# Kernel optimization log

Hardware: AMD Instinct MI355X
Metric: run time of the kernel (lower is better)

Reference implementation:

```python
import jax, jax.numpy as jnp
import numpy as np

N, D, M, H, L, FF = 24, 128, 9, 8, 2, 256
F = D // H  # head dim = 16


def _ln(x, g, b, eps=1e-5):
    mu = jnp.mean(x, -1, keepdims=True)
    var = jnp.mean((x - mu) ** 2, -1, keepdims=True)
    return (x - mu) * jax.lax.rsqrt(var + eps) * g + b


def _pos_encoding(T, d):
    pos = np.arange(T)[:, None].astype(np.float32)
    div = np.exp(np.arange(0, d, 2).astype(np.float32) * (-np.log(10000.0) / d))
    pe = np.zeros((T, d), np.float32)
    pe[:, 0::2] = np.sin(pos * div)
    pe[:, 1::2] = np.cos(pos * div)
    return jnp.asarray(pe)


def _forward(inputs, emb_W, emb_b, sa_Wq, sa_bq, sa_Wk, sa_bk, sa_Wv, sa_bv,
             ta_Wq, ta_bq, ta_Wk, ta_bk, ta_Wv, ta_bv, ta_Wo, ta_bo,
             ln_g, ln_b, lns_g, lns_b, ff_W1, ff_b1, ff_W2, ff_b2, fin_W, fin_b):
    B, T, _ = inputs.shape
    # joint embedding: per-joint linear M->D
    x4 = inputs.reshape(B, T, N, M)
    emb = jnp.einsum('btnm,nmd->btnd', x4, emb_W) + emb_b
    x = emb.reshape(B, T, N * D) + _pos_encoding(T, N * D)[None]
    x = x.transpose(1, 0, 2)  # (T, B, N*D)
    # faithful to source: float attn_mask = tril(ones, -1) is ADDED to scores in torch MHA
    mask = jnp.tril(jnp.ones((T, T), x.dtype), -1)
    inv_sF = 1.0 / np.sqrt(F).astype(np.float32)
    for l in range(L):
        xl = x.reshape(T, B, N, D)
        # ---- spatial attention: K,V shared across joints, Q per joint, per head ----
        Ksp = jnp.einsum('tbnd,hdf->tbhnf', xl, sa_Wk[l]) + sa_bk[l][:, None, :]
        Vsp = jnp.einsum('tbnd,hdf->tbhnf', xl, sa_Wv[l]) + sa_bv[l][:, None, :]
        Qsp = jnp.einsum('tbnd,hndf->tbhnf', xl, sa_Wq[l]) + sa_bq[l]
        Asp = jax.nn.softmax(jnp.einsum('tbhnf,tbhmf->tbhnm', Qsp, Ksp) * inv_sF, axis=-1)
        so = jnp.einsum('tbhnm,tbhmf->tbhnf', Asp, Vsp)
        spatial = so.transpose(0, 1, 3, 2, 4).reshape(T, B, N * D)  # concat heads per joint
        spatial = _ln(spatial + x, ln_g[l], ln_b[l])
        # ---- temporal attention: independent MHA per joint (batched over joints) ----
        q = (jnp.einsum('tbnd,nde->tbne', xl, ta_Wq[l]) + ta_bq[l]).reshape(T, B, N, H, F)
        k = (jnp.einsum('tbnd,nde->tbne', xl, ta_Wk[l]) + ta_bk[l]).reshape(T, B, N, H, F)
        v = (jnp.einsum('tbnd,nde->tbne', xl, ta_Wv[l]) + ta_bv[l]).reshape(T, B, N, H, F)
        sc = jnp.einsum('tbnhf,sbnhf->bnhts', q, k) * inv_sF + mask
        At = jax.nn.softmax(sc, axis=-1)
        to = jnp.einsum('bnhts,sbnhf->tbnhf', At, v).reshape(T, B, N, D)
        to = jnp.einsum('tbnd,nde->tbne', to, ta_Wo[l]) + ta_bo[l]
        temporal = _ln(to.reshape(T, B, N * D) + x, ln_g[l], ln_b[l])
        # ---- per-joint feed-forward + residual + small layernorm ----
        a = (spatial + temporal).reshape(T, B, N, D)
        ff = jax.nn.relu(jnp.einsum('tbnd,df->tbnf', a, ff_W1[l]) + ff_b1[l])
        ff = jnp.einsum('tbnf,fd->tbnd', ff, ff_W2[l]) + ff_b2[l]
        x = _ln(ff + a, lns_g[l], lns_b[l]).reshape(T, B, N * D)
    o = jnp.einsum('tbnd,dm->tbnm', x.reshape(T, B, N, D), fin_W) + fin_b
    return o.reshape(T, B, N * M).transpose(1, 0, 2) + inputs


def setup_inputs() -> dict:
    key = jax.random.key(0)
    ks = jax.random.split(key, 20)
    s = 0.05
    rn = lambda k, shape: jax.random.normal(k, shape, jnp.float32) * s
    return {
        'inputs': jax.random.normal(ks[0], (16, 192, N * M), jnp.float32),
        'emb_W': rn(ks[1], (N, M, D)), 'emb_b': rn(ks[2], (N, D)),
        'sa_Wq': rn(ks[3], (L, H, N, D, F)), 'sa_bq': rn(ks[4], (L, H, N, F)),
        'sa_Wk': rn(ks[5], (L, H, D, F)), 'sa_bk': rn(ks[6], (L, H, F)),
        'sa_Wv': rn(ks[7], (L, H, D, F)), 'sa_bv': rn(ks[8], (L, H, F)),
        'ta_Wq': rn(ks[9], (L, N, D, D)), 'ta_bq': rn(ks[10], (L, N, D)),
        'ta_Wk': rn(ks[11], (L, N, D, D)), 'ta_bk': rn(ks[12], (L, N, D)),
        'ta_Wv': rn(ks[13], (L, N, D, D)), 'ta_bv': rn(ks[14], (L, N, D)),
        'ta_Wo': rn(ks[15], (L, N, D, D)), 'ta_bo': jnp.zeros((L, N, D), jnp.float32),
        'ln_g': jnp.ones((L, N * D), jnp.float32), 'ln_b': jnp.zeros((L, N * D), jnp.float32),
        'lns_g': jnp.ones((L, D), jnp.float32), 'lns_b': jnp.zeros((L, D), jnp.float32),
        'ff_W1': rn(ks[16], (L, D, FF)), 'ff_b1': jnp.zeros((L, FF), jnp.float32),
        'ff_W2': rn(ks[17], (L, FF, D)), 'ff_b2': jnp.zeros((L, D), jnp.float32),
        'fin_W': rn(ks[18], (D, M)), 'fin_b': jnp.zeros((M,), jnp.float32),
    }


def reference(inputs, emb_W, emb_b, sa_Wq, sa_bq, sa_Wk, sa_bk, sa_Wv, sa_bv,
              ta_Wq, ta_bq, ta_Wk, ta_bk, ta_Wv, ta_bv, ta_Wo, ta_bo,
              ln_g, ln_b, lns_g, lns_b, ff_W1, ff_b1, ff_W2, ff_b2, fin_W, fin_b):
    return _forward(inputs, emb_W, emb_b, sa_Wq, sa_bq, sa_Wk, sa_bk, sa_Wv, sa_bv,
                    ta_Wq, ta_bq, ta_Wk, ta_bk, ta_Wv, ta_bv, ta_Wo, ta_bo,
                    ln_g, ln_b, lns_g, lns_b, ff_W1, ff_b1, ff_W2, ff_b2, fin_W, fin_b)
```

## Files before the change

### kernel.cpp

```cpp
#include <hip/hip_runtime.h>
#include <cmath>

namespace {
constexpr int B_ = 16, T_ = 192, N_ = 24, D_ = 128, M_ = 9, H_ = 8, F_ = 16, FF_ = 256;
constexpr int ND_ = N_ * D_;
constexpr int ROWS_ = T_ * B_;
constexpr long long SZ_ = (long long)ROWS_ * ND_;
constexpr long long WL_ = 2064384;
}

typedef __attribute__((ext_vector_type(8))) short bf16x8_t;
typedef __attribute__((ext_vector_type(4))) short bf16x4_t;
typedef __attribute__((ext_vector_type(4))) float f32x4_t;

static __device__ __forceinline__ ushort f2bf(float f) {
  union { float f; uint u; } v; v.f = f;
  uint r = v.u + 0x7fffu + ((v.u >> 16) & 1u);
  return (ushort)(r >> 16);
}
static __device__ __forceinline__ float bf2f(ushort u) {
  union { uint u; float f; } v; v.u = ((uint)u) << 16; return v.f;
}
static __device__ __forceinline__ bf16x4_t cvt4(f32x4_t x) {
  bf16x4_t r;
  r[0] = (short)f2bf(x[0]); r[1] = (short)f2bf(x[1]);
  r[2] = (short)f2bf(x[2]); r[3] = (short)f2bf(x[3]);
  return r;
}

__global__ __launch_bounds__(256) void k_pe(float* __restrict__ pe)
{
  int i = blockIdx.x * 256 + threadIdx.x;
  if (i >= T_ * ND_) return;
  int t = i / ND_, c = i % ND_;
  float freq = expf((float)(2 * (c >> 1)) * (-9.210340371976184f / 3072.0f));
  float ang = (float)t * freq;
  pe[i] = (c & 1) ? cosf(ang) : sinf(ang);
}

__global__ __launch_bounds__(256) void k_embed(const float* __restrict__ in,
                                               const float* __restrict__ Wemb,
                                               const float* __restrict__ bemb,
                                               const float* __restrict__ pe,
                                               ushort* __restrict__ Xb)
{
  int row = blockIdx.x;
  int t = row / B_, b = row % B_;
  int tid = threadIdx.x;
  __shared__ float inr[N_ * M_];
  const float* ip = in + ((size_t)b * T_ + t) * (N_ * M_);
  if (tid < N_ * M_) inr[tid] = ip[tid];
  __syncthreads();
  uint* Xr = (uint*)(Xb + (size_t)row * ND_);
  const float* per = pe + (size_t)t * ND_;
  for (int cc = tid; cc < ND_ / 2; cc += 256) {
    int c = cc * 2;
    int n = c >> 7;
    int d = c & 127;
    const float* xr = &inr[n * M_];
    float a0 = bemb[n * D_ + d] + per[c];
    float a1 = bemb[n * D_ + d + 1] + per[c + 1];
    const float* wp = Wemb + (size_t)(n * M_) * D_ + d;
    #pragma unroll
    for (int m = 0; m < M_; ++m) {
      float xm = xr[m];
      a0 += xm * wp[(size_t)m * D_];
      a1 += xm * wp[(size_t)m * D_ + 1];
    }
    Xr[cc] = (uint)f2bf(a0) | ((uint)f2bf(a1) << 16);
  }
}

__global__ __launch_bounds__(256) void k_pack_sp(const float* __restrict__ saWq,
                                                 const float* __restrict__ sabq,
                                                 const float* __restrict__ saWk,
                                                 const float* __restrict__ sabk,
                                                 const float* __restrict__ saWv,
                                                 const float* __restrict__ sabv,
                                                 ushort* __restrict__ wts,
                                                 float* __restrict__ fb)
{
  int l = blockIdx.y;
  int i = blockIdx.x * 256 + threadIdx.x;
  ushort* wl = wts + (long long)l * WL_;
  float* fl = fb + l * 3328;
  if (i < 393216) {
    int d = i & 127, e = (i >> 7) & 127, n = i >> 14;
    int h = e >> 4, f = e & 15;
    wl[i] = f2bf(saWq[(long long)l * 393216 + (((size_t)h * N_ + n) * D_ + d) * F_ + f]);
  } else if (i < 409600) {
    int j = i - 393216;
    int d = j & 127, e = j >> 7, h = e >> 4, f = e & 15;
    wl[i] = f2bf(saWk[(long long)l * 16384 + ((size_t)h * D_ + d) * F_ + f]);
  } else if (i < 425984) {
    int j = i - 409600;
    int d = j & 127, e = j >> 7, h = e >> 4, f = e & 15;
    wl[i] = f2bf(saWv[(long long)l * 16384 + ((size_t)h * D_ + d) * F_ + f]);
  } else if (i < 429056) {
    int j = i - 425984;
    int n = j >> 7, e = j & 127, h = e >> 4, f = e & 15;
    fl[j] = sabq[l * 3072 + ((size_t)h * N_ + n) * F_ + f];
  } else if (i < 429184) {
    int j = i - 429056, h = j >> 4, f = j & 15;
    fl[3072 + j] = sabk[l * 128 + h * F_ + f];
  } else if (i < 429312) {
    int j = i - 429184, h = j >> 4, f = j & 15;
    fl[3200 + j] = sabv[l * 128 + h * F_ + f];
  }
}

struct PackWArgs {
  const float* src[6];
  ushort* wts;
};
__global__ __launch_bounds__(256) void k_pack_w(PackWArgs args)
{
  __shared__ float tile[64][65];
  int l = blockIdx.y;
  int x = blockIdx.x;
  ushort* wl = args.wts + (long long)l * WL_;
  const float* sp; ushort* dp;
  int bx, by, Rr, Cc;
  if (x < 384) {
    int ten = x / 96, rem = x % 96, g = rem / 4, tl = rem % 4;
    bx = tl & 1; by = tl >> 1; Rr = 128; Cc = 128;
    sp = args.src[ten] + (long long)l * 393216 + (long long)g * 16384;
    dp = wl + 425984 + (long long)ten * 393216 + (long long)g * 16384;
  } else if (x < 392) {
    int idx = x - 384; bx = idx & 3; by = idx >> 2; Rr = 128; Cc = 256;
    sp = args.src[4] + (long long)l * 32768;
    dp = wl + 1998848;
  } else {
    int idx = x - 392; bx = idx & 1; by = idx >> 1; Rr = 256; Cc = 128;
    sp = args.src[5] + (long long)l * 32768;
    dp = wl + 2031616;
  }
  int c0 = bx * 64, r0 = by * 64;
  int ci = threadIdx.x & 63, rq = threadIdx.x >> 6;
  #pragma unroll
  for (int k = 0; k < 16; ++k) {
    int r = rq * 16 + k;
    tile[r][ci] = sp[(long long)(r0 + r) * Cc + c0 + ci];
  }
  __syncthreads();
  int ri = threadIdx.x & 63, cq = threadIdx.x >> 6;
  #pragma unroll
  for (int k = 0; k < 16; ++k) {
    int c = cq * 16 + k;
    dp[(long long)(c0 + c) * Rr + r0 + ri] = f2bf(tile[ri][c]);
  }
}

struct Qkv6Args {
  const ushort* W[6];
  const float* bias[6];
  ushort* C[6];
  long long wGroup[6];
  int biasGroup[6];
  int tpose[6];
};
__global__ __launch_bounds__(256) void k_qkv6(const ushort* __restrict__ A, Qkv6Args args)
{
  __shared__ ushort Wl[128][136];
  int p = blockIdx.y;
  int gz = blockIdx.z;
  int tid = threadIdx.x;
  int lane = tid & 63, wid = tid >> 6;
  int lr = lane & 15, lg = lane >> 4;
  int row0 = blockIdx.x * 64 + wid * 16;
  {
    const ushort* Wb = args.W[p] + (long long)gz * args.wGroup[p];
    int se = tid >> 4, sj = tid & 15;
    #pragma unroll
    for (int it = 0; it < 8; ++it) {
      uint4 v = *(const uint4*)(Wb + (it * 16 + se) * 128 + sj * 8);
      *(uint4*)&Wl[it * 16 + se][sj * 8] = v;
    }
  }
  union { bf16x8_t v; bf16x4_t h[2]; } au[4];
  {
    const ushort* ap = A + (long long)gz * 128 + (long long)(row0 + lr) * ND_ + lg * 4;
    #pragma unroll
    for (int kq = 0; kq < 4; ++kq) {
      au[kq].h[0] = *(const bf16x4_t*)(ap + kq * 32);
      au[kq].h[1] = *(const bf16x4_t*)(ap + kq * 32 + 16);
    }
  }
  __syncthreads();
  f32x4_t acc[8];
  #pragma unroll
  for (int n = 0; n < 8; ++n) acc[n] = (f32x4_t){0.f, 0.f, 0.f, 0.f};
  #pragma unroll
  for (int n = 0; n < 8; ++n) {
    int e = n * 16 + lr;
    #pragma unroll
    for (int kq = 0; kq < 4; ++kq) {
      union { bf16x8_t v; bf16x4_t h[2]; } bu;
      bu.h[0] = *(const bf16x4_t*)&Wl[e][kq * 32 + lg * 4];
      bu.h[1] = *(const bf16x4_t*)&Wl[e][kq * 32 + 16 + lg * 4];
      acc[n] = __builtin_amdgcn_mfma_f32_16x16x32_bf16(au[kq].v, bu.v, acc[n], 0, 0, 0);
    }
  }
  const float* bb = args.bias[p] + (long long)gz * args.biasGroup[p];
  if (args.tpose[p]) {
    ushort* Cp = args.C[p];
    #pragma unroll
    for (int n = 0; n < 8; ++n) {
      float bv = bb[n * 16 + lr];
      #pragma unroll
      for (int r = 0; r < 4; ++r) {
        int rg = row0 + lg * 4 + r;
        int tt = rg >> 4, bI = rg & 15;
        long long gI = ((long long)bI * N_ + gz) * H_ + n;
        Cp[(gI * T_ + tt) * F_ + lr] = f2bf(acc[n][r] + bv);
      }
    }
  } else {
    ushort* Cp = args.C[p] + (long long)gz * 128;
    #pragma unroll
    for (int n = 0; n < 8; ++n) {
      float bv = bb[n * 16 + lr];
      #pragma unroll
      for (int r = 0; r < 4; ++r)
        Cp[(long long)(row0 + lg * 4 + r) * ND_ + n * 16 + lr] = f2bf(acc[n][r] + bv);
    }
  }
}

__global__ __launch_bounds__(256) void k_ff1(
    const ushort* __restrict__ A, const ushort* __restrict__ Wt,
    const float* __restrict__ bias, ushort* __restrict__ Cout)
{
  __shared__ ushort Wl[128][136];
  int tid = threadIdx.x;
  int lane = tid & 63, wid = tid >> 6;
  int lr = lane & 15, lg = lane >> 4;
  int row0 = blockIdx.x * 64 + wid * 16;
  union { bf16x8_t v; bf16x4_t h[2]; } au[4];
  {
    const ushort* ap = A + (long long)(row0 + lr) * 128 + lg * 4;
    #pragma unroll
    for (int kq = 0; kq < 4; ++kq) {
      au[kq].h[0] = *(const bf16x4_t*)(ap + kq * 32);
      au[kq].h[1] = *(const bf16x4_t*)(ap + kq * 32 + 16);
    }
  }
  {
    const ushort* Wb = Wt + (long long)blockIdx.y * 128 * 128;
    int se = tid >> 4, sj = tid & 15;
    #pragma unroll
    for (int it = 0; it < 8; ++it) {
      uint4 v = *(const uint4*)(Wb + (it * 16 + se) * 128 + sj * 8);
      *(uint4*)&Wl[it * 16 + se][sj * 8] = v;
    }
  }
  __syncthreads();
  f32x4_t acc[8];
  #pragma unroll
  for (int n = 0; n < 8; ++n) acc[n] = (f32x4_t){0.f, 0.f, 0.f, 0.f};
  #pragma unroll
  for (int n = 0; n < 8; ++n) {
    int e = n * 16 + lr;
    #pragma unroll
    for (int kq = 0; kq < 4; ++kq) {
      union { bf16x8_t v; bf16x4_t h[2]; } bu;
      bu.h[0] = *(const bf16x4_t*)&Wl[e][kq * 32 + lg * 4];
      bu.h[1] = *(const bf16x4_t*)&Wl[e][kq * 32 + 16 + lg * 4];
      acc[n] = __builtin_amdgcn_mfma_f32_16x16x32_bf16(au[kq].v, bu.v, acc[n], 0, 0, 0);
    }
  }
  const float* bb = bias + blockIdx.y * 128;
  int ccolBase = blockIdx.y * 128 + lr;
  #pragma unroll
  for (int n = 0; n < 8; ++n) {
    float bv = bb[n * 16 + lr];
    #pragma unroll
    for (int r = 0; r < 4; ++r) {
      float v = fmaxf(acc[n][r] + bv, 0.f);
      Cout[(long long)(row0 + lg * 4 + r) * 256 + ccolBase + n * 16] = f2bf(v);
    }
  }
}

__global__ __launch_bounds__(256) void k_ff2_ln(
    const ushort* __restrict__ A,
    const ushort* __restrict__ Wt,
    const float* __restrict__ bias,
    const ushort* __restrict__ Res,
    const float* __restrict__ g,
    const float* __restrict__ be,
    ushort* __restrict__ Xb)
{
  __shared__ ushort Wl[128][264];
  int tid = threadIdx.x;
  int lane = tid & 63, wid = tid >> 6;
  int lr = lane & 15, lg = lane >> 4;
  int row0 = blockIdx.x * 64 + wid * 16;
  union { bf16x8_t v; bf16x4_t h[2]; } au[8];
  {
    const ushort* ap = A + (long long)(row0 + lr) * 256 + lg * 4;
    #pragma unroll
    for (int kq = 0; kq < 8; ++kq) {
      au[kq].h[0] = *(const bf16x4_t*)(ap + kq * 32);
      au[kq].h[1] = *(const bf16x4_t*)(ap + kq * 32 + 16);
    }
  }
  {
    #pragma unroll
    for (int it = 0; it < 16; ++it) {
      int idx = it * 256 + tid;
      int e = idx >> 5, j = idx & 31;
      uint4 v = *(const uint4*)(Wt + e * 256 + j * 8);
      *(uint4*)&Wl[e][j * 8] = v;
    }
  }
  __syncthreads();
  f32x4_t acc[8];
  #pragma unroll
  for (int n = 0; n < 8; ++n) acc[n] = (f32x4_t){0.f, 0.f, 0.f, 0.f};
  #pragma unroll
  for (int n = 0; n < 8; ++n) {
    int e = n * 16 + lr;
    #pragma unroll
    for (int kq = 0; kq < 8; ++kq) {
      union { bf16x8_t v; bf16x4_t h[2]; } bu;
      bu.h[0] = *(const bf16x4_t*)&Wl[e][kq * 32 + lg * 4];
      bu.h[1] = *(const bf16x4_t*)&Wl[e][kq * 32 + 16 + lg * 4];
      acc[n] = __builtin_amdgcn_mfma_f32_16x16x32_bf16(au[kq].v, bu.v, acc[n], 0, 0, 0);
    }
  }
  float s[4] = {0.f, 0.f, 0.f, 0.f};
  float s2[4] = {0.f, 0.f, 0.f, 0.f};
  #pragma unroll
  for (int n = 0; n < 8; ++n) {
    float bv = bias[n * 16 + lr];
    #pragma unroll
    for (int r = 0; r < 4; ++r) {
      float v = acc[n][r] + bv
              + bf2f(Res[(long long)(row0 + lg * 4 + r) * 128 + n * 16 + lr]);
      acc[n][r] = v;
      s[r] += v;
      s2[r] += v * v;
    }
  }
  #pragma unroll
  for (int m = 1; m < 16; m <<= 1) {
    #pragma unroll
    for (int r = 0; r < 4; ++r) {
      s[r] += __shfl_xor(s[r], m, 64);
      s2[r] += __shfl_xor(s2[r], m, 64);
    }
  }
  #pragma unroll
  for (int r = 0; r < 4; ++r) {
    float mu = s[r] * (1.f / 128.f);
    float var = s2[r] * (1.f / 128.f) - mu * mu;
    float rs = rsqrtf(var + 1e-5f);
    long long rb = (long long)(row0 + lg * 4 + r) * 128;
    #pragma unroll
    for (int n = 0; n < 8; ++n) {
      int col = n * 16 + lr;
      Xb[rb + col] = f2bf((acc[n][r] - mu) * rs * g[col] + be[col]);
    }
  }
}

__global__ __launch_bounds__(256) void k_oproj(const ushort* __restrict__ A,
                                               const ushort* __restrict__ Wt,
                                               const float* __restrict__ bias,
                                               ushort* __restrict__ Cout)
{
  __shared__ ushort Wl[128][136];
  int gz = blockIdx.z;
  int tid = threadIdx.x;
  int lane = tid & 63, wid = tid >> 6;
  int lr = lane & 15, lg = lane >> 4;
  int row0 = blockIdx.x * 64 + wid * 16;
  int tW = row0 >> 4;
  union { bf16x8_t v; bf16x4_t h[2]; } au[4];
  {
    const ushort* ab = A + (((long long)lr * N_ + gz) * H_) * ((long long)T_ * F_)
                         + (long long)tW * F_ + lg * 4;
    #pragma unroll
    for (int kq = 0; kq < 4; ++kq) {
      au[kq].h[0] = *(const bf16x4_t*)(ab + (long long)(2 * kq) * (T_ * F_));
      au[kq].h[1] = *(const bf16x4_t*)(ab + (long long)(2 * kq + 1) * (T_ * F_));
    }
  }
  {
    const ushort* Wb = Wt + (long long)gz * 16384;
    int se = tid >> 4, sj = tid & 15;
    #pragma unroll
    for (int it = 0; it < 8; ++it) {
      uint4 v = *(const uint4*)(Wb + (it * 16 + se) * 128 + sj * 8);
      *(uint4*)&Wl[it * 16 + se][sj * 8] = v;
    }
  }
  __syncthreads();
  f32x4_t acc[8];
  #pragma unroll
  for (int n = 0; n < 8; ++n) acc[n] = (f32x4_t){0.f, 0.f, 0.f, 0.f};
  #pragma unroll
  for (int n = 0; n < 8; ++n) {
    int e = n * 16 + lr;
    #pragma unroll
    for (int kq = 0; kq < 4; ++kq) {
      union { bf16x8_t v; bf16x4_t h[2]; } bu;
      bu.h[0] = *(const bf16x4_t*)&Wl[e][kq * 32 + lg * 4];
      bu.h[1] = *(const bf16x4_t*)&Wl[e][kq * 32 + 16 + lg * 4];
      acc[n] = __builtin_amdgcn_mfma_f32_16x16x32_bf16(au[kq].v, bu.v, acc[n], 0, 0, 0);
    }
  }
  const float* bb = bias + (long long)gz * 128;
  ushort* C = Cout + (long long)gz * 128;
  #pragma unroll
  for (int n = 0; n < 8; ++n) {
    float bv = bb[n * 16 + lr];
    #pragma unroll
    for (int r = 0; r < 4; ++r)
      C[(long long)(row0 + lg * 4 + r) * ND_ + n * 16 + lr] = f2bf(acc[n][r] + bv);
  }
}

__global__ __launch_bounds__(256) void k_spatial_ln(const ushort* __restrict__ Qg,
                                                    const ushort* __restrict__ Kg,
                                                    const ushort* __restrict__ Vg,
                                                    const ushort* __restrict__ Xb,
                                                    const float* __restrict__ g,
                                                    const float* __restrict__ be,
                                                    ushort* __restrict__ T2b)
{
  int row = blockIdx.x;
  int tid = threadIdx.x;
  __shared__ float Ks[8 * 409];
  __shared__ float Vs[8 * 409];
  __shared__ float ps[4], ps2[4];
  {
    const uint4* K4 = (const uint4*)(Kg + (size_t)row * ND_);
    const uint4* V4 = (const uint4*)(Vg + (size_t)row * ND_);
    for (int i8 = tid; i8 < 384; i8 += 256) {
      int n = i8 >> 4, e8 = (i8 & 15) * 8;
      int h = e8 >> 4, f0 = e8 & 15;
      int basei = h * 409 + n * 17 + f0;
      union { uint4 u; ushort s[8]; } kv, vv;
      kv.u = K4[i8];
      vv.u = V4[i8];
      #pragma unroll
      for (int j = 0; j < 8; ++j) {
        Ks[basei + j] = bf2f(kv.s[j]);
        Vs[basei + j] = bf2f(vv.s[j]);
      }
    }
  }
  __syncthreads();
  float o[F_];
  float s = 0.f, s2 = 0.f;
  int n = tid >> 3, h = tid & 7;
  int cbase = n * D_ + h * F_;
  if (tid < 192) {
    float q[F_];
    {
      const ushort* qp = Qg + (size_t)row * ND_ + cbase;
      union { uint4 u[2]; ushort s[16]; } qv;
      qv.u[0] = *(const uint4*)qp;
      qv.u[1] = *(const uint4*)(qp + 8);
      #pragma unroll
      for (int f = 0; f < F_; ++f) q[f] = bf2f(qv.s[f]);
    }
    float sc[N_];
    float mx = -1e30f;
    const float* Kh = &Ks[h * 409];
    for (int m = 0; m < N_; ++m) {
      float sd = 0.f;
      #pragma unroll
      for (int f = 0; f < F_; ++f) sd += q[f] * Kh[m * 17 + f];
      sd *= 0.25f;
      sc[m] = sd;
      mx = fmaxf(mx, sd);
    }
    float den = 0.f;
    for (int m = 0; m < N_; ++m) { sc[m] = __expf(sc[m] - mx); den += sc[m]; }
    float inv = 1.f / den;
    #pragma unroll
    for (int f = 0; f < F_; ++f) o[f] = 0.f;
    const float* Vh = &Vs[h * 409];
    for (int m = 0; m < N_; ++m) {
      float p = sc[m] * inv;
      #pragma unroll
      for (int f = 0; f < F_; ++f) o[f] += p * Vh[m * 17 + f];
    }
    {
      const ushort* xp = Xb + (size_t)row * ND_ + cbase;
      union { uint4 u[2]; ushort s[16]; } xu;
      xu.u[0] = *(const uint4*)xp;
      xu.u[1] = *(const uint4*)(xp + 8);
      #pragma unroll
      for (int f = 0; f < F_; ++f) {
        float v = o[f] + bf2f(xu.s[f]);
        o[f] = v;
        s += v;
        s2 += v * v;
      }
    }
  }
  #pragma unroll
  for (int m = 1; m < 64; m <<= 1) {
    s += __shfl_xor(s, m, 64);
    s2 += __shfl_xor(s2, m, 64);
  }
  int w = tid >> 6;
  if ((tid & 63) == 0) { ps[w] = s; ps2[w] = s2; }
  __syncthreads();
  float ts = ps[0] + ps[1] + ps[2] + ps[3];
  float ts2 = ps2[0] + ps2[1] + ps2[2] + ps2[3];
  float mu = ts / (float)ND_;
  float var = ts2 / (float)ND_ - mu * mu;
  float rs = rsqrtf(var + 1e-5f);
  if (tid < 192) {
    union { uint4 u[2]; ushort s[16]; } ov;
    #pragma unroll
    for (int f = 0; f < F_; ++f)
      ov.s[f] = f2bf((o[f] - mu) * rs * g[cbase + f] + be[cbase + f]);
    ushort* op = T2b + (size_t)row * ND_ + cbase;
    *(uint4*)op = ov.u[0];
    *(uint4*)(op + 8) = ov.u[1];
  }
}

__global__ __launch_bounds__(256) void k_temporal_mfma(const ushort* __restrict__ tQ,
                                                       const ushort* __restrict__ tK,
                                                       const ushort* __restrict__ tV,
                                                       ushort* __restrict__ Ob)
{
  long long gb = (long long)blockIdx.x * (T_ * F_);
  int tid = threadIdx.x;
  __shared__ ushort Kl[T_][20];
  __shared__ ushort Ql[T_][20];
  __shared__ ushort Vt[F_][200];
  {
    const uint4* Kg4 = (const uint4*)(tK + gb);
    const uint4* Qg4 = (const uint4*)(tQ + gb);
    const uint4* Vg4 = (const uint4*)(tV + gb);
    for (int task = tid; task < 1152; task += 256) {
      int ten = task / 384, idx = task - ten * 384;
      int t = idx >> 1, half = idx & 1;
      if (ten == 0) {
        uint4 v = Kg4[idx];
        *(uint2*)&Kl[t][half * 8] = make_uint2(v.x, v.y);
        *(uint2*)&Kl[t][half * 8 + 4] = make_uint2(v.z, v.w);
      } else if (ten == 1) {
        uint4 v = Qg4[idx];
        *(uint2*)&Ql[t][half * 8] = make_uint2(v.x, v.y);
        *(uint2*)&Ql[t][half * 8 + 4] = make_uint2(v.z, v.w);
      } else {
        union { uint4 u4; ushort s[8]; } vv;
        vv.u4 = Vg4[idx];
        #pragma unroll
        for (int f = 0; f < 8; ++f) Vt[half * 8 + f][t] = vv.s[f];
      }
    }
  }
  __syncthreads();
  int lane = tid & 63, wid = tid >> 6;
  int lr = lane & 15, lg = lane >> 4;
  const bf16x4_t z4 = (bf16x4_t){0, 0, 0, 0};
  const f32x4_t zf = (f32x4_t){0.f, 0.f, 0.f, 0.f};
  #pragma unroll
  for (int jj = 0; jj < 3; ++jj) {
    int q0 = (wid * 3 + jj) * 16;
    union { bf16x8_t v; bf16x4_t h4[2]; } qf;
    qf.h4[0] = *(const bf16x4_t*)&Ql[q0 + lr][lg * 4];
    qf.h4[1] = z4;
    f32x4_t d[12];
    #pragma unroll
    for (int i = 0; i < 12; ++i) {
      union { bf16x8_t v; bf16x4_t h4[2]; } kf;
      kf.h4[0] = *(const bf16x4_t*)&Kl[i * 16 + lr][lg * 4];
      kf.h4[1] = z4;
      d[i] = __builtin_amdgcn_mfma_f32_16x16x32_bf16(kf.v, qf.v, zf, 0, 0, 0);
    }
    int qg = q0 + lr;
    float lsum = 0.f;
    #pragma unroll
    for (int i = 0; i < 12; ++i) {
      #pragma unroll
      for (int r = 0; r < 4; ++r) {
        int k = i * 16 + lg * 4 + r;
        float p = __expf(d[i][r] * 0.25f + ((k < qg) ? 1.0f : 0.0f));
        d[i][r] = p;
        lsum += p;
      }
    }
    lsum += __shfl_xor(lsum, 16, 64);
    lsum += __shfl_xor(lsum, 32, 64);
    f32x4_t o = zf;
    #pragma unroll
    for (int i = 0; i < 6; ++i) {
      union { bf16x8_t v; bf16x4_t h4[2]; } vf;
      vf.h4[0] = *(const bf16x4_t*)&Vt[lr][i * 32 + lg * 4];
      vf.h4[1] = *(const bf16x4_t*)&Vt[lr][i * 32 + 16 + lg * 4];
      union { bf16x8_t v; bf16x4_t h4[2]; } pf;
      pf.h4[0] = cvt4(d[2 * i]);
      pf.h4[1] = cvt4(d[2 * i + 1]);
      o = __builtin_amdgcn_mfma_f32_16x16x32_bf16(vf.v, pf.v, o, 0, 0, 0);
    }
    float inv = 1.f / lsum;
    bf16x4_t ov;
    #pragma unroll
    for (int r = 0; r < 4; ++r) ov[r] = (short)f2bf(o[r] * inv);
    *(bf16x4_t*)(Ob + gb + (long long)qg * F_ + lg * 4) = ov;
  }
}

__global__ __launch_bounds__(256) void k_lnres_add(const ushort* __restrict__ Ain,
                                                   const ushort* __restrict__ Xb,
                                                   const ushort* __restrict__ T2,
                                                   const float* __restrict__ g,
                                                   const float* __restrict__ be,
                                                   ushort* __restrict__ Ab)
{
  int row = blockIdx.x;
  int tid = threadIdx.x;
  __shared__ float ps[4], ps2[4];
  const uint4* Ar = (const uint4*)(Ain + (size_t)row * ND_);
  const uint4* Xr = (const uint4*)(Xb + (size_t)row * ND_);
  float v0[8], v1[8];
  float s = 0.f, s2 = 0.f;
  {
    uint4 av = Ar[tid], xv = Xr[tid];
    const ushort* ap = (const ushort*)&av;
    const ushort* xp = (const ushort*)&xv;
    #pragma unroll
    for (int j = 0; j < 8; ++j) {
      float v = bf2f(ap[j]) + bf2f(xp[j]);
      v0[j] = v;
      s += v;
      s2 += v * v;
    }
  }
  if (tid < 128) {
    uint4 av = Ar[tid + 256], xv = Xr[tid + 256];
    const ushort* ap = (const ushort*)&av;
    const ushort* xp = (const ushort*)&xv;
    #pragma unroll
    for (int j = 0; j < 8; ++j) {
      float v = bf2f(ap[j]) + bf2f(xp[j]);
      v1[j] = v;
      s += v;
      s2 += v * v;
    }
  }
  #pragma unroll
  for (int m = 1; m < 64; m <<= 1) {
    s += __shfl_xor(s, m, 64);
    s2 += __shfl_xor(s2, m, 64);
  }
  int w = tid >> 6;
  if ((tid & 63) == 0) { ps[w] = s; ps2[w] = s2; }
  __syncthreads();
  float ts = ps[0] + ps[1] + ps[2] + ps[3];
  float ts2 = ps2[0] + ps2[1] + ps2[2] + ps2[3];
  float mu = ts / (float)ND_;
  float var = ts2 / (float)ND_ - mu * mu;
  float rs = rsqrtf(var + 1e-5f);
  const uint4* Tr = (const uint4*)(T2 + (size_t)row * ND_);
  uint4* Or = (uint4*)(Ab + (size_t)row * ND_);
  {
    uint4 tv = Tr[tid];
    const ushort* tp = (const ushort*)&tv;
    uint4 ov;
    ushort* op = (ushort*)&ov;
    int i0 = tid * 8;
    #pragma unroll
    for (int j = 0; j < 8; ++j)
      op[j] = f2bf((v0[j] - mu) * rs * g[i0 + j] + be[i0 + j] + bf2f(tp[j]));
    Or[tid] = ov;
  }
  if (tid < 128) {
    uint4 tv = Tr[tid + 256];
    const ushort* tp = (const ushort*)&tv;
    uint4 ov;
    ushort* op = (ushort*)&ov;
    int i0 = (tid + 256) * 8;
    #pragma unroll
    for (int j = 0; j < 8; ++j)
      op[j] = f2bf((v1[j] - mu) * rs * g[i0 + j] + be[i0 + j] + bf2f(tp[j]));
    Or[tid + 256] = ov;
  }
}

__global__ __launch_bounds__(256) void k_final(const ushort* __restrict__ Xb,
                                               const float* __restrict__ Wf,
                                               const float* __restrict__ bf,
                                               const float* __restrict__ in,
                                               float* __restrict__ out)
{
  int row = blockIdx.x;
  int t = row / B_, b = row % B_;
  int tid = threadIdx.x;
  __shared__ float xr[ND_];
  const uint4* Xr = (const uint4*)(Xb + (size_t)row * ND_);
  for (int i8 = tid; i8 < ND_ / 8; i8 += 256) {
    uint4 xv = Xr[i8];
    const ushort* xp = (const ushort*)&xv;
    #pragma unroll
    for (int j = 0; j < 8; ++j) xr[i8 * 8 + j] = bf2f(xp[j]);
  }
  __syncthreads();
  if (tid < N_ * M_) {
    int n = tid / M_, mm = tid % M_;
    float acc = bf[mm];
    for (int d = 0; d < D_; ++d) acc += xr[n * D_ + d] * Wf[(size_t)d * M_ + mm];
    size_t oi = ((size_t)b * T_ + t) * (N_ * M_) + tid;
    out[oi] = acc + in[oi];
  }
}

extern "C" void kernel_launch(void* const* d_in, const int* in_sizes, int n_in,
                              void* d_out, int out_size, void* d_ws, size_t ws_size,
                              hipStream_t stream)
{
  const float* inputs = (const float*)d_in[0];
  const float* emb_W  = (const float*)d_in[1];
  const float* emb_b  = (const float*)d_in[2];
  const float* sa_Wq  = (const float*)d_in[3];
  const float* sa_bq  = (const float*)d_in[4];
  const float* sa_Wk  = (const float*)d_in[5];
  const float* sa_bk  = (const float*)d_in[6];
  const float* sa_Wv  = (const float*)d_in[7];
  const float* sa_bv  = (const float*)d_in[8];
  const float* ta_Wq  = (const float*)d_in[9];
  const float* ta_bq  = (const float*)d_in[10];
  const float* ta_Wk  = (const float*)d_in[11];
  const float* ta_bk  = (const float*)d_in[12];
  const float* ta_Wv  = (const float*)d_in[13];
  const float* ta_bv  = (const float*)d_in[14];
  const float* ta_Wo  = (const float*)d_in[15];
  const float* ta_bo  = (const float*)d_in[16];
  const float* ln_g   = (const float*)d_in[17];
  const float* ln_b   = (const float*)d_in[18];
  const float* lns_g  = (const float*)d_in[19];
  const float* lns_b  = (const float*)d_in[20];
  const float* ff_W1  = (const float*)d_in[21];
  const float* ff_b1  = (const float*)d_in[22];
  const float* ff_W2  = (const float*)d_in[23];
  const float* ff_b2  = (const float*)d_in[24];
  const float* fin_W  = (const float*)d_in[25];
  const float* fin_b  = (const float*)d_in[26];
  float* out = (float*)d_out;

  char* base = (char*)d_ws;
  ushort* Xb  = (ushort*)base;
  ushort* C0  = (ushort*)(base + 2 * SZ_);
  ushort* T2b = (ushort*)(base + 14 * SZ_);
  ushort* sQ = C0;
  ushort* sK = C0 + SZ_;
  ushort* sV = C0 + 2 * SZ_;
  ushort* tQ = C0 + 3 * SZ_;
  ushort* tK = C0 + 4 * SZ_;
  ushort* tV = C0 + 5 * SZ_;
  ushort* AOb  = tV;
  ushort* Opjb = sQ;
  ushort* Ab   = sK;
  ushort* hB   = tK;

  ushort* wts = (ushort*)(base + 16 * SZ_);
  float* fb   = (float*)(wts + 2 * WL_);
  float* peT  = fb + 2 * 3328;

  k_pack_sp<<<dim3(1677, 2), 256, 0, stream>>>(sa_Wq, sa_bq, sa_Wk, sa_bk,
                                               sa_Wv, sa_bv, wts, fb);
  PackWArgs pw;
  pw.src[0] = ta_Wq; pw.src[1] = ta_Wk; pw.src[2] = ta_Wv; pw.src[3] = ta_Wo;
  pw.src[4] = ff_W1; pw.src[5] = ff_W2;
  pw.wts = wts;
  k_pack_w<<<dim3(400, 2), 256, 0, stream>>>(pw);

  k_pe<<<(T_ * ND_ + 255) / 256, 256, 0, stream>>>(peT);
  k_embed<<<ROWS_, 256, 0, stream>>>(inputs, emb_W, emb_b, peT, Xb);

  for (int l = 0; l < 2; ++l) {
    ushort* wl = wts + (long long)l * WL_;
    ushort* sWq = wl;
    ushort* sWk = wl + 393216;
    ushort* sWv = wl + 409600;
    ushort* tWq = wl + 425984;
    ushort* tWk = wl + 819200;
    ushort* tWv = wl + 1212416;
    ushort* tWo = wl + 1605632;
    ushort* W1t = wl + 1998848;
    ushort* W2t = wl + 2031616;
    float* fl = fb + l * 3328;
    float* bqP = fl;
    float* bkP = fl + 3072;
    float* bvP = fl + 3200;

    Qkv6Args qa;
    qa.W[0] = sWk; qa.bias[0] = bkP;                         qa.C[0] = sK;
    qa.wGroup[0] = 0;     qa.biasGroup[0] = 0;   qa.tpose[0] = 0;
    qa.W[1] = sWv; qa.bias[1] = bvP;                         qa.C[1] = sV;
    qa.wGroup[1] = 0;     qa.biasGroup[1] = 0;   qa.tpose[1] = 0;
    qa.W[2] = sWq; qa.bias[2] = bqP;                         qa.C[2] = sQ;
    qa.wGroup[2] = 16384; qa.biasGroup[2] = 128; qa.tpose[2] = 0;
    qa.W[3] = tWq; qa.bias[3] = ta_bq + (size_t)l * N_ * D_; qa.C[3] = tQ;
    qa.wGroup[3] = 16384; qa.biasGroup[3] = 128; qa.tpose[3] = 1;
    qa.W[4] = tWk; qa.bias[4] = ta_bk + (size_t)l * N_ * D_; qa.C[4] = tK;
    qa.wGroup[4] = 16384; qa.biasGroup[4] = 128; qa.tpose[4] = 1;
    qa.W[5] = tWv; qa.bias[5] = ta_bv + (size_t)l * N_ * D_; qa.C[5] = tV;
    qa.wGroup[5] = 16384; qa.biasGroup[5] = 128; qa.tpose[5] = 1;
    k_qkv6<<<dim3(ROWS_ / 64, 6, N_), 256, 0, stream>>>(Xb, qa);

    k_spatial_ln<<<ROWS_, 256, 0, stream>>>(sQ, sK, sV, Xb, ln_g + (size_t)l * ND_,
                                            ln_b + (size_t)l * ND_, T2b);

    k_temporal_mfma<<<B_ * N_ * H_, 256, 0, stream>>>(tQ, tK, tV, AOb);
    k_oproj<<<dim3(ROWS_ / 64, 1, N_), 256, 0, stream>>>(
        AOb, tWo, ta_bo + (size_t)l * N_ * D_, Opjb);

    k_lnres_add<<<ROWS_, 256, 0, stream>>>(Opjb, Xb, T2b, ln_g + (size_t)l * ND_,
                                           ln_b + (size_t)l * ND_, Ab);

    k_ff1<<<dim3(ROWS_ * N_ / 64, 2, 1), 256, 0, stream>>>(
        Ab, W1t, ff_b1 + (size_t)l * FF_, hB);
    k_ff2_ln<<<dim3(ROWS_ * N_ / 64, 1, 1), 256, 0, stream>>>(
        hB, W2t, ff_b2 + (size_t)l * D_, Ab,
        lns_g + (size_t)l * D_, lns_b + (size_t)l * D_, Xb);
  }

  k_final<<<ROWS_, 256, 0, stream>>>(Xb, fin_W, fin_b, inputs, out);
}
```

Before: 479.9 us.

## Pre-pack weights in MFMA fragment order and load directly from global

Weight packing kernels now write bf16 weights in the per-lane MFMA B-fragment order, so each lane's 8-element operand is contiguous. The GEMM kernels (qkv, ff1/ff2, oproj) drop the shared-memory weight staging and the __syncthreads, loading one 16-byte fragment per MFMA straight from global/L2. This removes LDS traffic, the barrier and shared memory use, which may raise occupancy. In exchange every wave re-reads the weights from cache instead of sharing one staged copy.

```diff
diff --git a/kernel.cpp b/kernel.cpp
--- a/kernel.cpp
+++ b/kernel.cpp
@@ -26,6 +26,13 @@
   r[0] = (short)f2bf(x[0]); r[1] = (short)f2bf(x[1]);
   r[2] = (short)f2bf(x[2]); r[3] = (short)f2bf(x[3]);
   return r;
+}
+static __device__ __forceinline__ int fragIdx(int e, int k, int KQ) {
+  int n = e >> 4, lr = e & 15;
+  int kq = k >> 5, krem = k & 31;
+  int hi = krem >> 4, rem = krem & 15;
+  int lg = rem >> 2, jj = rem & 3;
+  return (((n * KQ + kq) * 64 + lg * 16 + lr) << 3) + hi * 4 + jj;
 }
 
 __global__ __launch_bounds__(256) void k_pe(float* __restrict__ pe)
@@ -85,16 +92,37 @@
   ushort* wl = wts + (long long)l * WL_;
   float* fl = fb + l * 3328;
   if (i < 393216) {
-    int d = i & 127, e = (i >> 7) & 127, n = i >> 14;
+    int gz = i >> 14, il = i & 16383;
+    int j = il & 7;
+    int lane = (il >> 3) & 63;
+    int nk = il >> 9;
+    int kq = nk & 3, n8 = nk >> 2;
+    int lr = lane & 15, lg = lane >> 4;
+    int e = n8 * 16 + lr;
+    int d = kq * 32 + lg * 4 + (j & 3) + ((j >> 2) << 4);
     int h = e >> 4, f = e & 15;
-    wl[i] = f2bf(saWq[(long long)l * 393216 + (((size_t)h * N_ + n) * D_ + d) * F_ + f]);
+    wl[i] = f2bf(saWq[(long long)l * 393216 + (((size_t)h * N_ + gz) * D_ + d) * F_ + f]);
   } else if (i < 409600) {
-    int j = i - 393216;
-    int d = j & 127, e = j >> 7, h = e >> 4, f = e & 15;
+    int il = i - 393216;
+    int j = il & 7;
+    int lane = (il >> 3) & 63;
+    int nk = il >> 9;
+    int kq = nk & 3, n8 = nk >> 2;
+    int lr = lane & 15, lg = lane >> 4;
+    int e = n8 * 16 + lr;
+    int d = kq * 32 + lg * 4 + (j & 3) + ((j >> 2) << 4);
+    int h = e >> 4, f = e & 15;
     wl[i] = f2bf(saWk[(long long)l * 16384 + ((size_t)h * D_ + d) * F_ + f]);
   } else if (i < 425984) {
-    int j = i - 409600;
-    int d = j & 127, e = j >> 7, h = e >> 4, f = e & 15;
+    int il = i - 409600;
+    int j = il & 7;
+    int lane = (il >> 3) & 63;
+    int nk = il >> 9;
+    int kq = nk & 3, n8 = nk >> 2;
+    int lr = lane & 15, lg = lane >> 4;
+    int e = n8 * 16 + lr;
+    int d = kq * 32 + lg * 4 + (j & 3) + ((j >> 2) << 4);
+    int h = e >> 4, f = e & 15;
     wl[i] = f2bf(saWv[(long long)l * 16384 + ((size_t)h * D_ + d) * F_ + f]);
   } else if (i < 429056) {
     int j = i - 425984;
@@ -120,18 +148,18 @@
   int x = blockIdx.x;
   ushort* wl = args.wts + (long long)l * WL_;
   const float* sp; ushort* dp;
-  int bx, by, Rr, Cc;
+  int bx, by, Rr, Cc, mode;
   if (x < 384) {
     int ten = x / 96, rem = x % 96, g = rem / 4, tl = rem % 4;
-    bx = tl & 1; by = tl >> 1; Rr = 128; Cc = 128;
+    bx = tl & 1; by = tl >> 1; Rr = 128; Cc = 128; mode = 0;
     sp = args.src[ten] + (long long)l * 393216 + (long long)g * 16384;
     dp = wl + 425984 + (long long)ten * 393216 + (long long)g * 16384;
   } else if (x < 392) {
-    int idx = x - 384; bx = idx & 3; by = idx >> 2; Rr = 128; Cc = 256;
+    int idx = x - 384; bx = idx & 3; by = idx >> 2; Rr = 128; Cc = 256; mode = 1;
     sp = args.src[4] + (long long)l * 32768;
     dp = wl + 1998848;
   } else {
-    int idx = x - 392; bx = idx & 1; by = idx >> 1; Rr = 256; Cc = 128;
+    int idx = x - 392; bx = idx & 1; by = idx >> 1; Rr = 256; Cc = 128; mode = 2;
     sp = args.src[5] + (long long)l * 32768;
     dp = wl + 2031616;
   }
@@ -147,7 +175,13 @@
   #pragma unroll
   for (int k = 0; k < 16; ++k) {
     int c = cq * 16 + k;
-    dp[(long long)(c0 + c) * Rr + r0 + ri] = f2bf(tile[ri][c]);
+    int eg = c0 + c;
+    int kg = r0 + ri;
+    int idx;
+    if (mode == 1)      idx = (eg >> 7) * 16384 + fragIdx(eg & 127, kg, 4);
+    else if (mode == 2) idx = fragIdx(eg, kg, 8);
+    else                idx = fragIdx(eg, kg, 4);
+    dp[idx] = f2bf(tile[ri][c]);
   }
 }
 
@@ -161,22 +195,13 @@
 };
 __global__ __launch_bounds__(256) void k_qkv6(const ushort* __restrict__ A, Qkv6Args args)
 {
-  __shared__ ushort Wl[128][136];
   int p = blockIdx.y;
   int gz = blockIdx.z;
   int tid = threadIdx.x;
   int lane = tid & 63, wid = tid >> 6;
   int lr = lane & 15, lg = lane >> 4;
   int row0 = blockIdx.x * 64 + wid * 16;
-  {
-    const ushort* Wb = args.W[p] + (long long)gz * args.wGroup[p];
-    int se = tid >> 4, sj = tid & 15;
-    #pragma unroll
-    for (int it = 0; it < 8; ++it) {
-      uint4 v = *(const uint4*)(Wb + (it * 16 + se) * 128 + sj * 8);
-      *(uint4*)&Wl[it * 16 + se][sj * 8] = v;
-    }
-  }
+  const ushort* Wf = args.W[p] + (long long)gz * args.wGroup[p];
   union { bf16x8_t v; bf16x4_t h[2]; } au[4];
   {
     const ushort* ap = A + (long long)gz * 128 + (long long)(row0 + lr) * ND_ + lg * 4;
@@ -186,19 +211,15 @@
       au[kq].h[1] = *(const bf16x4_t*)(ap + kq * 32 + 16);
     }
   }
-  __syncthreads();
   f32x4_t acc[8];
   #pragma unroll
   for (int n = 0; n < 8; ++n) acc[n] = (f32x4_t){0.f, 0.f, 0.f, 0.f};
   #pragma unroll
   for (int n = 0; n < 8; ++n) {
-    int e = n * 16 + lr;
     #pragma unroll
     for (int kq = 0; kq < 4; ++kq) {
-      union { bf16x8_t v; bf16x4_t h[2]; } bu;
-      bu.h[0] = *(const bf16x4_t*)&Wl[e][kq * 32 + lg * 4];
-      bu.h[1] = *(const bf16x4_t*)&Wl[e][kq * 32 + 16 + lg * 4];
-      acc[n] = __builtin_amdgcn_mfma_f32_16x16x32_bf16(au[kq].v, bu.v, acc[n], 0, 0, 0);
+      bf16x8_t bu = *(const bf16x8_t*)(Wf + (((n * 4 + kq) * 64 + lane) << 3));
+      acc[n] = __builtin_amdgcn_mfma_f32_16x16x32_bf16(au[kq].v, bu, acc[n], 0, 0, 0);
     }
   }
   const float* bb = args.bias[p] + (long long)gz * args.biasGroup[p];
@@ -231,11 +252,11 @@
     const ushort* __restrict__ A, const ushort* __restrict__ Wt,
     const float* __restrict__ bias, ushort* __restrict__ Cout)
 {
-  __shared__ ushort Wl[128][136];
   int tid = threadIdx.x;
   int lane = tid & 63, wid = tid >> 6;
   int lr = lane & 15, lg = lane >> 4;
   int row0 = blockIdx.x * 64 + wid * 16;
+  const ushort* Wf = Wt + (long long)blockIdx.y * 16384;
   union { bf16x8_t v; bf16x4_t h[2]; } au[4];
   {
     const ushort* ap = A + (long long)(row0 + lr) * 128 + lg * 4;
@@ -245,28 +266,15 @@
       au[kq].h[1] = *(const bf16x4_t*)(ap + kq * 32 + 16);
     }
   }
-  {
-    const ushort* Wb = Wt + (long long)blockIdx.y * 128 * 128;
-    int se = tid >> 4, sj = tid & 15;
-    #pragma unroll
-    for (int it = 0; it < 8; ++it) {
-      uint4 v = *(const uint4*)(Wb + (it * 16 + se) * 128 + sj * 8);
-      *(uint4*)&Wl[it * 16 + se][sj * 8] = v;
-    }
-  }
-  __syncthreads();
   f32x4_t acc[8];
   #pragma unroll
   for (int n = 0; n < 8; ++n) acc[n] = (f32x4_t){0.f, 0.f, 0.f, 0.f};
   #pragma unroll
   for (int n = 0; n < 8; ++n) {
-    int e = n * 16 + lr;
     #pragma unroll
     for (int kq = 0; kq < 4; ++kq) {
-      union { bf16x8_t v; bf16x4_t h[2]; } bu;
-      bu.h[0] = *(const bf16x4_t*)&Wl[e][kq * 32 + lg * 4];
-      bu.h[1] = *(const bf16x4_t*)&Wl[e][kq * 32 + 16 + lg * 4];
-      acc[n] = __builtin_amdgcn_mfma_f32_16x16x32_bf16(au[kq].v, bu.v, acc[n], 0, 0, 0);
+      bf16x8_t bu = *(const bf16x8_t*)(Wf + (((n * 4 + kq) * 64 + lane) << 3));
+      acc[n] = __builtin_amdgcn_mfma_f32_16x16x32_bf16(au[kq].v, bu, acc[n], 0, 0, 0);
     }
   }
   const float* bb = bias + blockIdx.y * 128;
@@ -291,7 +299,6 @@
     const float* __restrict__ be,
     ushort* __restrict__ Xb)
 {
-  __shared__ ushort Wl[128][264];
   int tid = threadIdx.x;
   int lane = tid & 63, wid = tid >> 6;
   int lr = lane & 15, lg = lane >> 4;
@@ -305,28 +312,15 @@
       au[kq].h[1] = *(const bf16x4_t*)(ap + kq * 32 + 16);
     }
   }
-  {
-    #pragma unroll
-    for (int it = 0; it < 16; ++it) {
-      int idx = it * 256 + tid;
-      int e = idx >> 5, j = idx & 31;
-      uint4 v = *(const uint4*)(Wt + e * 256 + j * 8);
-      *(uint4*)&Wl[e][j * 8] = v;
-    }
-  }
-  __syncthreads();
   f32x4_t acc[8];
   #pragma unroll
   for (int n = 0; n < 8; ++n) acc[n] = (f32x4_t){0.f, 0.f, 0.f, 0.f};
   #pragma unroll
   for (int n = 0; n < 8; ++n) {
-    int e = n * 16 + lr;
     #pragma unroll
     for (int kq = 0; kq < 8; ++kq) {
-      union { bf16x8_t v; bf16x4_t h[2]; } bu;
-      bu.h[0] = *(const bf16x4_t*)&Wl[e][kq * 32 + lg * 4];
-      bu.h[1] = *(const bf16x4_t*)&Wl[e][kq * 32 + 16 + lg * 4];
-      acc[n] = __builtin_amdgcn_mfma_f32_16x16x32_bf16(au[kq].v, bu.v, acc[n], 0, 0, 0);
+      bf16x8_t bu = *(const bf16x8_t*)(Wt + (((n * 8 + kq) * 64 + lane) << 3));
+      acc[n] = __builtin_amdgcn_mfma_f32_16x16x32_bf16(au[kq].v, bu, acc[n], 0, 0, 0);
     }
   }
   float s[4] = {0.f, 0.f, 0.f, 0.f};
@@ -370,13 +364,13 @@
                                                const float* __restrict__ bias,
                                                ushort* __restrict__ Cout)
 {
-  __shared__ ushort Wl[128][136];
   int gz = blockIdx.z;
   int tid = threadIdx.x;
   int lane = tid & 63, wid = tid >> 6;
   int lr = lane & 15, lg = lane >> 4;
   int row0 = blockIdx.x * 64 + wid * 16;
   int tW = row0 >> 4;
+  const ushort* Wf = Wt + (long long)gz * 16384;
   union { bf16x8_t v; bf16x4_t h[2]; } au[4];
   {
     const ushort* ab = A + (((long long)lr * N_ + gz) * H_) * ((long long)T_ * F_)
@@ -387,28 +381,15 @@
       au[kq].h[1] = *(const bf16x4_t*)(ab + (long long)(2 * kq + 1) * (T_ * F_));
     }
   }
-  {
-    const ushort* Wb = Wt + (long long)gz * 16384;
-    int se = tid >> 4, sj = tid & 15;
-    #pragma unroll
-    for (int it = 0; it < 8; ++it) {
-      uint4 v = *(const uint4*)(Wb + (it * 16 + se) * 128 + sj * 8);
-      *(uint4*)&Wl[it * 16 + se][sj * 8] = v;
-    }
-  }
-  __syncthreads();
   f32x4_t acc[8];
   #pragma unroll
   for (int n = 0; n < 8; ++n) acc[n] = (f32x4_t){0.f, 0.f, 0.f, 0.f};
   #pragma unroll
   for (int n = 0; n < 8; ++n) {
-    int e = n * 16 + lr;
     #pragma unroll
     for (int kq = 0; kq < 4; ++kq) {
-      union { bf16x8_t v; bf16x4_t h[2]; } bu;
-      bu.h[0] = *(const bf16x4_t*)&Wl[e][kq * 32 + lg * 4];
-      bu.h[1] = *(const bf16x4_t*)&Wl[e][kq * 32 + 16 + lg * 4];
-      acc[n] = __builtin_amdgcn_mfma_f32_16x16x32_bf16(au[kq].v, bu.v, acc[n], 0, 0, 0);
+      bf16x8_t bu = *(const bf16x8_t*)(Wf + (((n * 4 + kq) * 64 + lane) << 3));
+      acc[n] = __builtin_amdgcn_mfma_f32_16x16x32_bf16(au[kq].v, bu, acc[n], 0, 0, 0);
     }
   }
   const float* bb = bias + (long long)gz * 128;
```

New measurement: 535.8 us. 11.6% more time.
